# Kernel optimization log

Measured on AMD Instinct MI355X. Metric: run time of the kernel, lower is better.

## Reference

```python
import jax, jax.numpy as jnp
import numpy as np

N_NODES = 100000

def _sage_conv(x, edge_index, W_l, b_l, W_r):
    # PyG SAGEConv default: mean-aggregate neighbor (source) features at dst,
    # then out = lin_l(agg) + lin_r(x). lin_l has bias, lin_r does not.
    src, dst = edge_index[0], edge_index[1]
    msg = x[src]                                   # [E, F]
    summed = jax.ops.segment_sum(msg, dst, num_segments=N_NODES)  # [N, F]
    cnt = jax.ops.segment_sum(jnp.ones((src.shape[0],), x.dtype), dst,
                              num_segments=N_NODES)
    agg = summed / jnp.maximum(cnt, 1.0)[:, None]
    return agg @ W_l + b_l + x @ W_r


def setup_inputs() -> dict:
    key = jax.random.key(0)
    ks = jax.random.split(key, 10)
    F_IN, H, C = 128, 16, 8
    E = 3200000
    x = jax.random.normal(ks[0], (N_NODES, F_IN), dtype=jnp.float32)
    edge_index = jax.random.randint(ks[1], (2, E), 0, N_NODES, dtype=jnp.int64)
    s1 = 1.0 / np.sqrt(F_IN)
    s2 = 1.0 / np.sqrt(H)
    sc = 1.0 / np.sqrt(2 * H)
    return {
        "x": x,
        "edge_index": edge_index,
        "W1_l": jax.random.uniform(ks[2], (F_IN, H), jnp.float32, -s1, s1),
        "b1": jnp.zeros((H,), jnp.float32),
        "W1_r": jax.random.uniform(ks[3], (F_IN, H), jnp.float32, -s1, s1),
        "W2_l": jax.random.uniform(ks[4], (H, H), jnp.float32, -s2, s2),
        "b2": jnp.zeros((H,), jnp.float32),
        "W2_r": jax.random.uniform(ks[5], (H, H), jnp.float32, -s2, s2),
        "Wc": jax.random.uniform(ks[6], (2 * H, C), jnp.float32, -sc, sc),
        "bc": jax.random.uniform(ks[7], (C,), jnp.float32, -sc, sc),
    }


def reference(x, edge_index, W1_l, b1, W1_r, W2_l, b2, W2_r, Wc, bc):
    h = jax.nn.relu(_sage_conv(x, edge_index, W1_l, b1, W1_r))
    # F.dropout(training=False) in eval mode -> identity
    h = jax.nn.relu(_sage_conv(h, edge_index, W2_l, b2, W2_r))
    edge_feat = jnp.concatenate([h[edge_index[0]], h[edge_index[1]]], axis=-1)  # [E, 32]
    logits = edge_feat @ Wc + bc                                                # [E, C]
    return jax.nn.log_softmax(logits, axis=1)
```

## Files before the change

kernel.cpp:

```cpp
#include <hip/hip_runtime.h>
#include <hip/hip_bf16.h>
#include <hip/hip_fp16.h>


#define NBLK 512
#define BUCKET_BITS 9
#define BUCKET_SZ 512
#define MAXNB 256
#define STAGE_CAP 18000

struct __align__(16) H8 { __half2 a, b, c, d; };

__global__ __launch_bounds__(512) void prep_kernel(const int* __restrict__ ei,
                                                   int* __restrict__ counts,
                                                   const float* __restrict__ x,
                                                   const float* __restrict__ W1l,
                                                   const float* __restrict__ W1r,
                                                   __half* __restrict__ yh,
                                                   float* __restrict__ z,
                                                   int E, int N, int NB, int chunk,
                                                   int nbin) {
  __shared__ float smem[64 * 129 + 128 * 32];
  int t = threadIdx.x;
  if ((int)blockIdx.x < nbin) {
    int* hist = (int*)smem;
    for (int i = t; i < NB; i += 512) hist[i] = 0;
    __syncthreads();
    int s = blockIdx.x * chunk;
    int eend = s + chunk; if (eend > E) eend = E;
    for (int e = s + t; e < eend; e += 512)
      atomicAdd(&hist[ei[E + e] >> BUCKET_BITS], 1);
    __syncthreads();
    for (int b = t; b < NB; b += 512)
      counts[b * NBLK + blockIdx.x] = hist[b];
  } else {
    float* Xs = smem;
    float* Ws = smem + 64 * 129;
    int nb = ((int)blockIdx.x - nbin) * 64;
    for (int i = t; i < 128 * 16; i += 512) {
      int kk = i >> 4, c = i & 15;
      Ws[kk * 32 + c] = W1l[i];
      Ws[kk * 32 + 16 + c] = W1r[i];
    }
    const float4* xg = (const float4*)(x + (size_t)nb * 128);
    for (int i4 = t; i4 < 64 * 32; i4 += 512) {
      int r = i4 >> 5, c4 = (i4 & 31) * 4;
      float4 val = make_float4(0.f, 0.f, 0.f, 0.f);
      if (nb + r < N) val = xg[i4];
      float* dp = &Xs[r * 129 + c4];
      dp[0] = val.x; dp[1] = val.y; dp[2] = val.z; dp[3] = val.w;
    }
    __syncthreads();
    int n = t & 63, cg = t >> 6;
    float a0 = 0.f, a1 = 0.f, a2 = 0.f, a3 = 0.f;
    for (int kk = 0; kk < 128; ++kk) {
      float xv = Xs[n * 129 + kk];
      const float* wr = &Ws[kk * 32 + cg * 4];
      a0 += xv * wr[0]; a1 += xv * wr[1]; a2 += xv * wr[2]; a3 += xv * wr[3];
    }
    int node = nb + n;
    if (node < N) {
      int c = cg * 4;
      if (c < 16) {
        __half2* yp = (__half2*)(yh + (size_t)node * 16 + c);
        yp[0] = __floats2half2_rn(a0, a1);
        yp[1] = __floats2half2_rn(a2, a3);
      } else {
        float* op = z + (size_t)node * 16 + (c - 16);
        op[0] = a0; op[1] = a1; op[2] = a2; op[3] = a3;
      }
    }
  }
}

__global__ __launch_bounds__(512) void scan1_kernel(const int* __restrict__ counts,
                                                    int* __restrict__ locoff,
                                                    int* __restrict__ total) {
  __shared__ int wsum[8];
  int b = blockIdx.x;
  int t = threadIdx.x;
  int lane = t & 63, wid = t >> 6;
  int v = counts[b * NBLK + t];
  int incl = v;
#pragma unroll
  for (int d = 1; d < 64; d <<= 1) {
    int u = __shfl_up(incl, d);
    if (lane >= d) incl += u;
  }
  if (lane == 63) wsum[wid] = incl;
  __syncthreads();
  if (t < 64) {
    int w = (t < 8) ? wsum[t] : 0;
#pragma unroll
    for (int d = 1; d < 8; d <<= 1) {
      int u = __shfl_up(w, d);
      if (lane >= d) w += u;
    }
    if (t < 8) wsum[t] = w;
  }
  __syncthreads();
  int excl = ((wid > 0) ? wsum[wid - 1] : 0) + (incl - v);
  locoff[b * NBLK + t] = excl;
  if (t == NBLK - 1) total[b] = excl + v;
}

__global__ __launch_bounds__(512) void binwrite_kernel(const int* __restrict__ ei,
                                                       const int* __restrict__ locoff,
                                                       const int* __restrict__ total,
                                                       int* __restrict__ elist,
                                                       int E, int NB, int chunk) {
  __shared__ int cur[MAXNB];
  __shared__ int ws4[4];
  int t = threadIdx.x;
  int lane = t & 63, wid = t >> 6;
  int v = (t < 256 && t < NB) ? total[t] : 0;
  int incl = v;
#pragma unroll
  for (int d = 1; d < 64; d <<= 1) {
    int u = __shfl_up(incl, d);
    if (lane >= d) incl += u;
  }
  if (t < 256 && lane == 63) ws4[wid] = incl;
  __syncthreads();
  if (t < 64) {
    int w = (t < 4) ? ws4[t] : 0;
#pragma unroll
    for (int d = 1; d < 4; d <<= 1) {
      int u = __shfl_up(w, d);
      if (lane >= d) w += u;
    }
    if (t < 4) ws4[t] = w;
  }
  __syncthreads();
  if (t < 256 && t < NB)
    cur[t] = ((wid > 0) ? ws4[wid - 1] : 0) + (incl - v) + locoff[t * NBLK + blockIdx.x];
  __syncthreads();
  int s = blockIdx.x * chunk;
  int eend = s + chunk; if (eend > E) eend = E;
  for (int e = s + t; e < eend; e += 512) {
    int src = ei[e];
    int dst = ei[E + e];
    int b = dst >> BUCKET_BITS;
    int pos = atomicAdd(&cur[b], 1);
    elist[pos] = ((dst & (BUCKET_SZ - 1)) << 17) | src;
  }
}

__global__ __launch_bounds__(1024) void sortagg_kernel(int* __restrict__ elist,
                                                       const int* __restrict__ total,
                                                       int* __restrict__ row_csr,
                                                       const __half* __restrict__ yh,
                                                       const float* __restrict__ z,
                                                       const float* __restrict__ b1,
                                                       const float* __restrict__ W2l,
                                                       const float* __restrict__ W2r,
                                                       __half* __restrict__ ph,
                                                       float* __restrict__ q,
                                                       int N, int NB) {
  extern __shared__ int sm[];
  int* stage  = sm;
  int* sorted = sm + STAGE_CAP;
  int* hist   = sm + 2 * STAGE_CAP;
  int* wtmp   = hist + 512;
  float* Wl_s = (float*)(wtmp + 16);
  float* Wr_s = Wl_s + 256;
  float* b_s  = Wr_s + 256;
  __shared__ int beg_s;
  int t = threadIdx.x;
  int b = blockIdx.x;
  int lane = t & 63, wid = t >> 6;
  if (t < 256) { Wl_s[t] = W2l[t]; Wr_s[t] = W2r[t]; }
  else if (t < 272) b_s[t - 256] = b1[t - 256];
  {
    int v = (t < 256 && t < NB) ? total[t] : 0;
    int incl = v;
#pragma unroll
    for (int d = 1; d < 64; d <<= 1) {
      int u = __shfl_up(incl, d);
      if (lane >= d) incl += u;
    }
    if (t < 256 && lane == 63) wtmp[wid] = incl;
    __syncthreads();
    if (t < 64) {
      int w = (t < 4) ? wtmp[t] : 0;
#pragma unroll
      for (int d = 1; d < 4; d <<= 1) {
        int u = __shfl_up(w, d);
        if (lane >= d) w += u;
      }
      if (t < 4) wtmp[t] = w;
    }
    __syncthreads();
    if (t == b) beg_s = ((wid > 0) ? wtmp[wid - 1] : 0) + (incl - v);
    __syncthreads();
  }
  int beg = beg_s;
  int cnt = total[b];
  if (cnt > STAGE_CAP) cnt = STAGE_CAP;
  for (int i = t; i < cnt; i += 1024) stage[i] = elist[beg + i];
  if (t < 512) hist[t] = 0;
  __syncthreads();
  for (int i = t; i < cnt; i += 1024)
    atomicAdd(&hist[((unsigned)stage[i]) >> 17], 1);
  __syncthreads();
  {
    int v = (t < 512) ? hist[t] : 0;
    int incl = v;
#pragma unroll
    for (int d = 1; d < 64; d <<= 1) {
      int u = __shfl_up(incl, d);
      if (lane >= d) incl += u;
    }
    if (t < 512 && lane == 63) wtmp[wid] = incl;
    __syncthreads();
    if (t < 64) {
      int w = (t < 8) ? wtmp[t] : 0;
#pragma unroll
      for (int d = 1; d < 8; d <<= 1) {
        int u = __shfl_up(w, d);
        if (lane >= d) w += u;
      }
      if (t < 8) wtmp[t] = w;
    }
    __syncthreads();
    if (t < 512) {
      int excl = ((wid > 0) ? wtmp[wid - 1] : 0) + (incl - v);
      hist[t] = excl;
      int node = (b << BUCKET_BITS) + t;
      if (node <= N) row_csr[node] = beg + excl;
    }
  }
  __syncthreads();
  for (int i = t; i < cnt; i += 1024) {
    unsigned ent = (unsigned)stage[i];
    int pos = atomicAdd(&hist[ent >> 17], 1);
    sorted[pos] = ent & 0x1FFFF;
  }
  __syncthreads();
  for (int i = t; i < cnt; i += 1024) elist[beg + i] = sorted[i];
  const __half2* yh2 = (const __half2*)yh;
  int base = b << BUCKET_BITS;
  int k = t & 7;
#pragma unroll
  for (int pass = 0; pass < 4; ++pass) {
    int dl = pass * 128 + (t >> 3);
    int node = base + dl;
    if (node < N) {
      int rbeg = dl ? hist[dl - 1] : 0;
      int rend = hist[dl];
      float a0 = 0.f, a1 = 0.f;
      int j = rbeg;
      for (; j + 4 <= rend; j += 4) {
        int s0 = sorted[j], s1 = sorted[j + 1];
        int s2 = sorted[j + 2], s3 = sorted[j + 3];
        float2 v0 = __half22float2(yh2[(size_t)s0 * 8 + k]);
        float2 v1 = __half22float2(yh2[(size_t)s1 * 8 + k]);
        float2 v2 = __half22float2(yh2[(size_t)s2 * 8 + k]);
        float2 v3 = __half22float2(yh2[(size_t)s3 * 8 + k]);
        a0 += v0.x + v1.x + v2.x + v3.x;
        a1 += v0.y + v1.y + v2.y + v3.y;
      }
      for (; j < rend; ++j) {
        float2 v = __half22float2(yh2[(size_t)sorted[j] * 8 + k]);
        a0 += v.x; a1 += v.y;
      }
      int deg = rend - rbeg;
      float inv = 1.f / (float)(deg > 0 ? deg : 1);
      float2 zv = ((const float2*)z)[(size_t)node * 8 + k];
      float h0 = fmaxf(a0 * inv + b_s[2 * k]     + zv.x, 0.f);
      float h1 = fmaxf(a1 * inv + b_s[2 * k + 1] + zv.y, 0.f);
      float pa0 = 0.f, pa1 = 0.f, qa0 = 0.f, qa1 = 0.f;
      int c0 = 2 * k;
#pragma unroll
      for (int kk2 = 0; kk2 < 8; ++kk2) {
        float ha = __shfl(h0, kk2, 8);
        float hb = __shfl(h1, kk2, 8);
        int r0 = 2 * kk2 * 16, r1 = r0 + 16;
        pa0 += ha * Wl_s[r0 + c0]     + hb * Wl_s[r1 + c0];
        pa1 += ha * Wl_s[r0 + c0 + 1] + hb * Wl_s[r1 + c0 + 1];
        qa0 += ha * Wr_s[r0 + c0]     + hb * Wr_s[r1 + c0];
        qa1 += ha * Wr_s[r0 + c0 + 1] + hb * Wr_s[r1 + c0 + 1];
      }
      ((__half2*)ph)[(size_t)node * 8 + k] = __floats2half2_rn(pa0, pa1);
      ((float2*)q)[(size_t)node * 8 + k] = make_float2(qa0, qa1);
    }
  }
}

__global__ __launch_bounds__(256) void agg2_kernel(const __half* __restrict__ ph,
                                                   const float* __restrict__ q,
                                                   const int* __restrict__ row_csr,
                                                   const int* __restrict__ srclist,
                                                   const float* __restrict__ b2,
                                                   const float* __restrict__ Wc,
                                                   __half* __restrict__ Uh,
                                                   __half* __restrict__ Vh, int N) {
  __shared__ float Wc_s[256], b_s[16];
  int t = threadIdx.x;
  if (t < 256) Wc_s[t] = Wc[t];
  if (t < 16) b_s[t] = b2[t];
  __syncthreads();
  int g = (blockIdx.x * 256 + t) >> 3;
  int k = t & 7;
  if (g >= N) return;
  int beg = row_csr[g], end = row_csr[g + 1];
  const __half2* ph2 = (const __half2*)ph;
  float a0 = 0.f, a1 = 0.f;
  int j = beg;
  for (; j + 4 <= end; j += 4) {
    int s0 = srclist[j], s1 = srclist[j + 1];
    int s2 = srclist[j + 2], s3 = srclist[j + 3];
    float2 v0 = __half22float2(ph2[(size_t)s0 * 8 + k]);
    float2 v1 = __half22float2(ph2[(size_t)s1 * 8 + k]);
    float2 v2 = __half22float2(ph2[(size_t)s2 * 8 + k]);
    float2 v3 = __half22float2(ph2[(size_t)s3 * 8 + k]);
    a0 += v0.x + v1.x + v2.x + v3.x;
    a1 += v0.y + v1.y + v2.y + v3.y;
  }
  for (; j < end; ++j) {
    float2 v = __half22float2(ph2[(size_t)srclist[j] * 8 + k]);
    a0 += v.x; a1 += v.y;
  }
  int deg = end - beg;
  float inv = 1.f / (float)(deg > 0 ? deg : 1);
  float2 qv = ((const float2*)q)[(size_t)g * 8 + k];
  float h0 = fmaxf(a0 * inv + b_s[2 * k]     + qv.x, 0.f);
  float h1 = fmaxf(a1 * inv + b_s[2 * k + 1] + qv.y, 0.f);
  int wb = (k < 4) ? 0 : 128;
  int c0 = 2 * (k & 3);
  float o0 = 0.f, o1 = 0.f;
#pragma unroll
  for (int kk2 = 0; kk2 < 8; ++kk2) {
    float ha = __shfl(h0, kk2, 8);
    float hb = __shfl(h1, kk2, 8);
    int r0 = wb + 2 * kk2 * 8, r1 = r0 + 8;
    o0 += ha * Wc_s[r0 + c0]     + hb * Wc_s[r1 + c0];
    o1 += ha * Wc_s[r0 + c0 + 1] + hb * Wc_s[r1 + c0 + 1];
  }
  __half2 o = __floats2half2_rn(o0, o1);
  if (k < 4) ((__half2*)Uh)[(size_t)g * 4 + k] = o;
  else       ((__half2*)Vh)[(size_t)g * 4 + (k - 4)] = o;
}

__global__ __launch_bounds__(256) void edge_out_kernel(const int* __restrict__ ei,
                                                       const __half* __restrict__ Uh,
                                                       const __half* __restrict__ Vh,
                                                       const float* __restrict__ bc,
                                                       float* __restrict__ out, int E) {
  int base = blockIdx.x * 1024 + threadIdx.x;
  float4 c0 = ((const float4*)bc)[0], c1 = ((const float4*)bc)[1];
  int s[4], d[4];
#pragma unroll
  for (int ii = 0; ii < 4; ++ii) {
    int e = base + ii * 256;
    s[ii] = (e < E) ? __builtin_nontemporal_load(ei + e) : 0;
    d[ii] = (e < E) ? __builtin_nontemporal_load(ei + E + e) : 0;
  }
  H8 u8[4], v8[4];
#pragma unroll
  for (int ii = 0; ii < 4; ++ii) {
    u8[ii] = *(const H8*)(Uh + (size_t)s[ii] * 8);
    v8[ii] = *(const H8*)(Vh + (size_t)d[ii] * 8);
  }
#pragma unroll
  for (int ii = 0; ii < 4; ++ii) {
    int e = base + ii * 256;
    if (e >= E) continue;
    float2 ua = __half22float2(u8[ii].a), ub = __half22float2(u8[ii].b);
    float2 uc = __half22float2(u8[ii].c), ud = __half22float2(u8[ii].d);
    float2 va = __half22float2(v8[ii].a), vb = __half22float2(v8[ii].b);
    float2 vc = __half22float2(v8[ii].c), vd = __half22float2(v8[ii].d);
    float tv[8];
    tv[0] = ua.x + va.x + c0.x; tv[1] = ua.y + va.y + c0.y;
    tv[2] = ub.x + vb.x + c0.z; tv[3] = ub.y + vb.y + c0.w;
    tv[4] = uc.x + vc.x + c1.x; tv[5] = uc.y + vc.y + c1.y;
    tv[6] = ud.x + vd.x + c1.z; tv[7] = ud.y + vd.y + c1.w;
    float m = tv[0];
#pragma unroll
    for (int c = 1; c < 8; ++c) m = fmaxf(m, tv[c]);
    float ssum = 0.f;
#pragma unroll
    for (int c = 0; c < 8; ++c) ssum += __expf(tv[c] - m);
    float lse = m + __logf(ssum);
    float4 o0 = make_float4(tv[0] - lse, tv[1] - lse, tv[2] - lse, tv[3] - lse);
    float4 o1 = make_float4(tv[4] - lse, tv[5] - lse, tv[6] - lse, tv[7] - lse);
    float4* op = (float4*)(out + (size_t)e * 8);
    op[0] = o0; op[1] = o1;
  }
}

extern "C" void kernel_launch(void* const* d_in, const int* in_sizes, int n_in,
                              void* d_out, int out_size, void* d_ws, size_t ws_size,
                              hipStream_t stream) {
  const float* x   = (const float*)d_in[0];
  const int*   ei  = (const int*)d_in[1];
  const float* W1l = (const float*)d_in[2];
  const float* b1  = (const float*)d_in[3];
  const float* W1r = (const float*)d_in[4];
  const float* W2l = (const float*)d_in[5];
  const float* b2  = (const float*)d_in[6];
  const float* W2r = (const float*)d_in[7];
  const float* Wc  = (const float*)d_in[8];
  const float* bc  = (const float*)d_in[9];
  float* out = (float*)d_out;

  const int N = in_sizes[0] / 128;
  const int E = in_sizes[1] / 2;
  const size_t N16 = (size_t)N * 16;
  const int NB = (N + BUCKET_SZ - 1) >> BUCKET_BITS;
  const int chunk = (E + NBLK - 1) / NBLK;

  __half* yh = (__half*)d_ws;
  __half* ph = yh + N16;
  __half* Uh = ph + N16;
  __half* Vh = Uh + (size_t)N * 8;
  float*  z  = (float*)(Vh + (size_t)N * 8);
  float*  q  = z + N16;
  int* counts  = (int*)(q + N16);
  int* locoff  = counts + NB * NBLK;
  int* total   = locoff + NB * NBLK;
  int* elist   = total + NB;
  int* row_csr = elist + E;

  int lin1_blocks = (N + 63) / 64;
  prep_kernel<<<NBLK + lin1_blocks, 512, 0, stream>>>(ei, counts, x, W1l, W1r,
                                                      yh, z, E, N, NB, chunk, NBLK);
  scan1_kernel<<<NB, 512, 0, stream>>>(counts, locoff, total);
  binwrite_kernel<<<NBLK, 512, 0, stream>>>(ei, locoff, total, elist, E, NB, chunk);

  size_t smem = (2 * STAGE_CAP + 512 + 16) * sizeof(int) + 528 * sizeof(float);
  sortagg_kernel<<<NB, 1024, smem, stream>>>(elist, total, row_csr, yh, z, b1,
                                             W2l, W2r, ph, q, N, NB);

  int ngrid = (N * 8 + 255) / 256;
  agg2_kernel<<<ngrid, 256, 0, stream>>>(ph, q, row_csr, elist, b2, Wc, Uh, Vh, N);

  int egrid = (E + 1023) / 1024;
  edge_out_kernel<<<egrid, 256, 0, stream>>>(ei, Uh, Vh, bc, out, E);
}
```

Before: 188.7 us.

## Replace global count-scan binning with fixed-capacity buckets and atomic cursors

Removes the separate histogram pass and scan1 kernel. Each destination bucket now gets a fixed-capacity slot of CAP entries, and binwrite reserves space per bucket with one global atomicAdd per block after computing a local histogram. Buckets are halved to 256 nodes so more sortagg blocks run with smaller shared memory, and a row_end array replaces the contiguous CSR offsets. edge_out also processes 8 edges per thread instead of 4. The costs are a larger elist allocation and silent truncation if any bucket exceeds CAP, which depends on the input degree distribution.

Measured after the change: 219.6 us. +16.4%, slower.

```diff
diff --git a/kernel.cpp b/kernel.cpp
--- a/kernel.cpp
+++ b/kernel.cpp
@@ -4,139 +4,82 @@
 
 
 #define NBLK 512
-#define BUCKET_BITS 9
-#define BUCKET_SZ 512
-#define MAXNB 256
-#define STAGE_CAP 18000
+#define BUCKET_BITS 8
+#define BUCKET_SZ 256
+#define CAP 9216
+#define MAXNB 512
 
 struct __align__(16) H8 { __half2 a, b, c, d; };
 
-__global__ __launch_bounds__(512) void prep_kernel(const int* __restrict__ ei,
-                                                   int* __restrict__ counts,
-                                                   const float* __restrict__ x,
+__global__ __launch_bounds__(512) void prep_kernel(const float* __restrict__ x,
                                                    const float* __restrict__ W1l,
                                                    const float* __restrict__ W1r,
                                                    __half* __restrict__ yh,
                                                    float* __restrict__ z,
-                                                   int E, int N, int NB, int chunk,
-                                                   int nbin) {
-  __shared__ float smem[64 * 129 + 128 * 32];
+                                                   int* __restrict__ gcur,
+                                                   int N, int NB, int nlin) {
   int t = threadIdx.x;
-  if ((int)blockIdx.x < nbin) {
-    int* hist = (int*)smem;
-    for (int i = t; i < NB; i += 512) hist[i] = 0;
-    __syncthreads();
-    int s = blockIdx.x * chunk;
-    int eend = s + chunk; if (eend > E) eend = E;
-    for (int e = s + t; e < eend; e += 512)
-      atomicAdd(&hist[ei[E + e] >> BUCKET_BITS], 1);
-    __syncthreads();
-    for (int b = t; b < NB; b += 512)
-      counts[b * NBLK + blockIdx.x] = hist[b];
-  } else {
-    float* Xs = smem;
-    float* Ws = smem + 64 * 129;
-    int nb = ((int)blockIdx.x - nbin) * 64;
-    for (int i = t; i < 128 * 16; i += 512) {
-      int kk = i >> 4, c = i & 15;
-      Ws[kk * 32 + c] = W1l[i];
-      Ws[kk * 32 + 16 + c] = W1r[i];
-    }
-    const float4* xg = (const float4*)(x + (size_t)nb * 128);
-    for (int i4 = t; i4 < 64 * 32; i4 += 512) {
-      int r = i4 >> 5, c4 = (i4 & 31) * 4;
-      float4 val = make_float4(0.f, 0.f, 0.f, 0.f);
-      if (nb + r < N) val = xg[i4];
-      float* dp = &Xs[r * 129 + c4];
-      dp[0] = val.x; dp[1] = val.y; dp[2] = val.z; dp[3] = val.w;
-    }
-    __syncthreads();
-    int n = t & 63, cg = t >> 6;
-    float a0 = 0.f, a1 = 0.f, a2 = 0.f, a3 = 0.f;
-    for (int kk = 0; kk < 128; ++kk) {
-      float xv = Xs[n * 129 + kk];
-      const float* wr = &Ws[kk * 32 + cg * 4];
-      a0 += xv * wr[0]; a1 += xv * wr[1]; a2 += xv * wr[2]; a3 += xv * wr[3];
-    }
-    int node = nb + n;
-    if (node < N) {
-      int c = cg * 4;
-      if (c < 16) {
-        __half2* yp = (__half2*)(yh + (size_t)node * 16 + c);
-        yp[0] = __floats2half2_rn(a0, a1);
-        yp[1] = __floats2half2_rn(a2, a3);
-      } else {
-        float* op = z + (size_t)node * 16 + (c - 16);
-        op[0] = a0; op[1] = a1; op[2] = a2; op[3] = a3;
-      }
-    }
-  }
-}
-
-__global__ __launch_bounds__(512) void scan1_kernel(const int* __restrict__ counts,
-                                                    int* __restrict__ locoff,
-                                                    int* __restrict__ total) {
-  __shared__ int wsum[8];
-  int b = blockIdx.x;
-  int t = threadIdx.x;
-  int lane = t & 63, wid = t >> 6;
-  int v = counts[b * NBLK + t];
-  int incl = v;
-#pragma unroll
-  for (int d = 1; d < 64; d <<= 1) {
-    int u = __shfl_up(incl, d);
-    if (lane >= d) incl += u;
-  }
-  if (lane == 63) wsum[wid] = incl;
-  __syncthreads();
-  if (t < 64) {
-    int w = (t < 8) ? wsum[t] : 0;
-#pragma unroll
-    for (int d = 1; d < 8; d <<= 1) {
-      int u = __shfl_up(w, d);
-      if (lane >= d) w += u;
-    }
-    if (t < 8) wsum[t] = w;
-  }
-  __syncthreads();
-  int excl = ((wid > 0) ? wsum[wid - 1] : 0) + (incl - v);
-  locoff[b * NBLK + t] = excl;
-  if (t == NBLK - 1) total[b] = excl + v;
+  if ((int)blockIdx.x == nlin) {
+    for (int b = t; b < NB; b += 512) gcur[b] = b * CAP;
+    return;
+  }
+  __shared__ float Xs[64 * 129];
+  __shared__ float Ws[128 * 32];
+  int nb = (int)blockIdx.x * 64;
+  for (int i = t; i < 128 * 16; i += 512) {
+    int kk = i >> 4, c = i & 15;
+    Ws[kk * 32 + c] = W1l[i];
+    Ws[kk * 32 + 16 + c] = W1r[i];
+  }
+  const float4* xg = (const float4*)(x + (size_t)nb * 128);
+  for (int i4 = t; i4 < 64 * 32; i4 += 512) {
+    int r = i4 >> 5, c4 = (i4 & 31) * 4;
+    float4 val = make_float4(0.f, 0.f, 0.f, 0.f);
+    if (nb + r < N) val = xg[i4];
+    float* dp = &Xs[r * 129 + c4];
+    dp[0] = val.x; dp[1] = val.y; dp[2] = val.z; dp[3] = val.w;
+  }
+  __syncthreads();
+  int n = t & 63, cg = t >> 6;
+  float a0 = 0.f, a1 = 0.f, a2 = 0.f, a3 = 0.f;
+  for (int kk = 0; kk < 128; ++kk) {
+    float xv = Xs[n * 129 + kk];
+    const float* wr = &Ws[kk * 32 + cg * 4];
+    a0 += xv * wr[0]; a1 += xv * wr[1]; a2 += xv * wr[2]; a3 += xv * wr[3];
+  }
+  int node = nb + n;
+  if (node < N) {
+    int c = cg * 4;
+    if (c < 16) {
+      __half2* yp = (__half2*)(yh + (size_t)node * 16 + c);
+      yp[0] = __floats2half2_rn(a0, a1);
+      yp[1] = __floats2half2_rn(a2, a3);
+    } else {
+      float* op = z + (size_t)node * 16 + (c - 16);
+      op[0] = a0; op[1] = a1; op[2] = a2; op[3] = a3;
+    }
+  }
 }
 
 __global__ __launch_bounds__(512) void binwrite_kernel(const int* __restrict__ ei,
-                                                       const int* __restrict__ locoff,
-                                                       const int* __restrict__ total,
+                                                       int* __restrict__ gcur,
                                                        int* __restrict__ elist,
                                                        int E, int NB, int chunk) {
+  __shared__ int hist[MAXNB];
   __shared__ int cur[MAXNB];
-  __shared__ int ws4[4];
   int t = threadIdx.x;
-  int lane = t & 63, wid = t >> 6;
-  int v = (t < 256 && t < NB) ? total[t] : 0;
-  int incl = v;
-#pragma unroll
-  for (int d = 1; d < 64; d <<= 1) {
-    int u = __shfl_up(incl, d);
-    if (lane >= d) incl += u;
-  }
-  if (t < 256 && lane == 63) ws4[wid] = incl;
-  __syncthreads();
-  if (t < 64) {
-    int w = (t < 4) ? ws4[t] : 0;
-#pragma unroll
-    for (int d = 1; d < 4; d <<= 1) {
-      int u = __shfl_up(w, d);
-      if (lane >= d) w += u;
-    }
-    if (t < 4) ws4[t] = w;
-  }
-  __syncthreads();
-  if (t < 256 && t < NB)
-    cur[t] = ((wid > 0) ? ws4[wid - 1] : 0) + (incl - v) + locoff[t * NBLK + blockIdx.x];
+  for (int i = t; i < NB; i += 512) hist[i] = 0;
   __syncthreads();
   int s = blockIdx.x * chunk;
   int eend = s + chunk; if (eend > E) eend = E;
+  for (int e = s + t; e < eend; e += 512)
+    atomicAdd(&hist[ei[E + e] >> BUCKET_BITS], 1);
+  __syncthreads();
+  for (int i = t; i < NB; i += 512) {
+    int c = hist[i];
+    cur[i] = c ? atomicAdd(&gcur[i], c) : 0;
+  }
+  __syncthreads();
   for (int e = s + t; e < eend; e += 512) {
     int src = ei[e];
     int dst = ei[E + e];
@@ -147,32 +90,40 @@
 }
 
 __global__ __launch_bounds__(1024) void sortagg_kernel(int* __restrict__ elist,
-                                                       const int* __restrict__ total,
+                                                       const int* __restrict__ gcur,
                                                        int* __restrict__ row_csr,
+                                                       int* __restrict__ row_end,
                                                        const __half* __restrict__ yh,
                                                        const float* __restrict__ z,
                                                        const float* __restrict__ b1,
                                                        const float* __restrict__ W2l,
                                                        const float* __restrict__ W2r,
                                                        __half* __restrict__ ph,
-                                                       float* __restrict__ q,
-                                                       int N, int NB) {
+                                                       float* __restrict__ q, int N) {
   extern __shared__ int sm[];
   int* stage  = sm;
-  int* sorted = sm + STAGE_CAP;
-  int* hist   = sm + 2 * STAGE_CAP;
-  int* wtmp   = hist + 512;
-  float* Wl_s = (float*)(wtmp + 16);
+  int* sorted = sm + CAP;
+  int* hist   = sm + 2 * CAP;
+  int* wtmp   = hist + 256;
+  float* Wl_s = (float*)(wtmp + 4);
   float* Wr_s = Wl_s + 256;
   float* b_s  = Wr_s + 256;
-  __shared__ int beg_s;
   int t = threadIdx.x;
   int b = blockIdx.x;
   int lane = t & 63, wid = t >> 6;
   if (t < 256) { Wl_s[t] = W2l[t]; Wr_s[t] = W2r[t]; }
   else if (t < 272) b_s[t - 256] = b1[t - 256];
+  int beg = b * CAP;
+  int cnt = gcur[b] - beg;
+  if (cnt > CAP) cnt = CAP;
+  for (int i = t; i < cnt; i += 1024) stage[i] = elist[beg + i];
+  if (t < 256) hist[t] = 0;
+  __syncthreads();
+  for (int i = t; i < cnt; i += 1024)
+    atomicAdd(&hist[((unsigned)stage[i]) >> 17], 1);
+  __syncthreads();
   {
-    int v = (t < 256 && t < NB) ? total[t] : 0;
+    int v = (t < 256) ? hist[t] : 0;
     int incl = v;
 #pragma unroll
     for (int d = 1; d < 64; d <<= 1) {
@@ -191,43 +142,11 @@
       if (t < 4) wtmp[t] = w;
     }
     __syncthreads();
-    if (t == b) beg_s = ((wid > 0) ? wtmp[wid - 1] : 0) + (incl - v);
-    __syncthreads();
-  }
-  int beg = beg_s;
-  int cnt = total[b];
-  if (cnt > STAGE_CAP) cnt = STAGE_CAP;
-  for (int i = t; i < cnt; i += 1024) stage[i] = elist[beg + i];
-  if (t < 512) hist[t] = 0;
-  __syncthreads();
-  for (int i = t; i < cnt; i += 1024)
-    atomicAdd(&hist[((unsigned)stage[i]) >> 17], 1);
-  __syncthreads();
-  {
-    int v = (t < 512) ? hist[t] : 0;
-    int incl = v;
-#pragma unroll
-    for (int d = 1; d < 64; d <<= 1) {
-      int u = __shfl_up(incl, d);
-      if (lane >= d) incl += u;
-    }
-    if (t < 512 && lane == 63) wtmp[wid] = incl;
-    __syncthreads();
-    if (t < 64) {
-      int w = (t < 8) ? wtmp[t] : 0;
-#pragma unroll
-      for (int d = 1; d < 8; d <<= 1) {
-        int u = __shfl_up(w, d);
-        if (lane >= d) w += u;
-      }
-      if (t < 8) wtmp[t] = w;
-    }
-    __syncthreads();
-    if (t < 512) {
+    if (t < 256) {
       int excl = ((wid > 0) ? wtmp[wid - 1] : 0) + (incl - v);
       hist[t] = excl;
       int node = (b << BUCKET_BITS) + t;
-      if (node <= N) row_csr[node] = beg + excl;
+      if (node < N) row_csr[node] = beg + excl;
     }
   }
   __syncthreads();
@@ -237,12 +156,16 @@
     sorted[pos] = ent & 0x1FFFF;
   }
   __syncthreads();
+  if (t < 256) {
+    int node = (b << BUCKET_BITS) + t;
+    if (node < N) row_end[node] = beg + hist[t];
+  }
   for (int i = t; i < cnt; i += 1024) elist[beg + i] = sorted[i];
   const __half2* yh2 = (const __half2*)yh;
   int base = b << BUCKET_BITS;
   int k = t & 7;
 #pragma unroll
-  for (int pass = 0; pass < 4; ++pass) {
+  for (int pass = 0; pass < 2; ++pass) {
     int dl = pass * 128 + (t >> 3);
     int node = base + dl;
     if (node < N) {
@@ -290,6 +213,7 @@
 __global__ __launch_bounds__(256) void agg2_kernel(const __half* __restrict__ ph,
                                                    const float* __restrict__ q,
                                                    const int* __restrict__ row_csr,
+                                                   const int* __restrict__ row_end,
                                                    const int* __restrict__ srclist,
                                                    const float* __restrict__ b2,
                                                    const float* __restrict__ Wc,
@@ -303,7 +227,7 @@
   int g = (blockIdx.x * 256 + t) >> 3;
   int k = t & 7;
   if (g >= N) return;
-  int beg = row_csr[g], end = row_csr[g + 1];
+  int beg = row_csr[g], end = row_end[g];
   const __half2* ph2 = (const __half2*)ph;
   float a0 = 0.f, a1 = 0.f;
   int j = beg;
@@ -342,28 +266,29 @@
   else       ((__half2*)Vh)[(size_t)g * 4 + (k - 4)] = o;
 }
 
+#define EIL 8
 __global__ __launch_bounds__(256) void edge_out_kernel(const int* __restrict__ ei,
                                                        const __half* __restrict__ Uh,
                                                        const __half* __restrict__ Vh,
                                                        const float* __restrict__ bc,
                                                        float* __restrict__ out, int E) {
-  int base = blockIdx.x * 1024 + threadIdx.x;
+  int base = blockIdx.x * (256 * EIL) + threadIdx.x;
   float4 c0 = ((const float4*)bc)[0], c1 = ((const float4*)bc)[1];
-  int s[4], d[4];
-#pragma unroll
-  for (int ii = 0; ii < 4; ++ii) {
+  int s[EIL], d[EIL];
+#pragma unroll
+  for (int ii = 0; ii < EIL; ++ii) {
     int e = base + ii * 256;
     s[ii] = (e < E) ? __builtin_nontemporal_load(ei + e) : 0;
     d[ii] = (e < E) ? __builtin_nontemporal_load(ei + E + e) : 0;
   }
-  H8 u8[4], v8[4];
-#pragma unroll
-  for (int ii = 0; ii < 4; ++ii) {
+  H8 u8[EIL], v8[EIL];
+#pragma unroll
+  for (int ii = 0; ii < EIL; ++ii) {
     u8[ii] = *(const H8*)(Uh + (size_t)s[ii] * 8);
     v8[ii] = *(const H8*)(Vh + (size_t)d[ii] * 8);
   }
 #pragma unroll
-  for (int ii = 0; ii < 4; ++ii) {
+  for (int ii = 0; ii < EIL; ++ii) {
     int e = base + ii * 256;
     if (e >= E) continue;
     float2 ua = __half22float2(u8[ii].a), ub = __half22float2(u8[ii].b);
@@ -416,25 +341,24 @@
   __half* Vh = Uh + (size_t)N * 8;
   float*  z  = (float*)(Vh + (size_t)N * 8);
   float*  q  = z + N16;
-  int* counts  = (int*)(q + N16);
-  int* locoff  = counts + NB * NBLK;
-  int* total   = locoff + NB * NBLK;
-  int* elist   = total + NB;
-  int* row_csr = elist + E;
+  int* gcur    = (int*)(q + N16);
+  int* elist   = gcur + NB;
+  int* row_csr = elist + (size_t)NB * CAP;
+  int* row_end = row_csr + N;
 
   int lin1_blocks = (N + 63) / 64;
-  prep_kernel<<<NBLK + lin1_blocks, 512, 0, stream>>>(ei, counts, x, W1l, W1r,
-                                                      yh, z, E, N, NB, chunk, NBLK);
-  scan1_kernel<<<NB, 512, 0, stream>>>(counts, locoff, total);
-  binwrite_kernel<<<NBLK, 512, 0, stream>>>(ei, locoff, total, elist, E, NB, chunk);
-
-  size_t smem = (2 * STAGE_CAP + 512 + 16) * sizeof(int) + 528 * sizeof(float);
-  sortagg_kernel<<<NB, 1024, smem, stream>>>(elist, total, row_csr, yh, z, b1,
-                                             W2l, W2r, ph, q, N, NB);
+  prep_kernel<<<lin1_blocks + 1, 512, 0, stream>>>(x, W1l, W1r, yh, z, gcur,
+                                                   N, NB, lin1_blocks);
+  binwrite_kernel<<<NBLK, 512, 0, stream>>>(ei, gcur, elist, E, NB, chunk);
+
+  size_t smem = (2 * CAP + 256 + 4) * sizeof(int) + 528 * sizeof(float);
+  sortagg_kernel<<<NB, 1024, smem, stream>>>(elist, gcur, row_csr, row_end,
+                                             yh, z, b1, W2l, W2r, ph, q, N);
 
   int ngrid = (N * 8 + 255) / 256;
-  agg2_kernel<<<ngrid, 256, 0, stream>>>(ph, q, row_csr, elist, b2, Wc, Uh, Vh, N);
-
-  int egrid = (E + 1023) / 1024;
+  agg2_kernel<<<ngrid, 256, 0, stream>>>(ph, q, row_csr, row_end, elist,
+                                         b2, Wc, Uh, Vh, N);
+
+  int egrid = (E + 256 * EIL - 1) / (256 * EIL);
   edge_out_kernel<<<egrid, 256, 0, stream>>>(ei, Uh, Vh, bc, out, E);
 }
```
